# Performance work log

Measured on AMD Instinct MI355X. Metric: run time of the kernel, lower is better.

The kernel has to match this reference:

```python
import jax, jax.numpy as jnp
import numpy as np

NEG = -1.0e9


def setup_inputs() -> dict:
    key = jax.random.key(0)
    ks = jax.random.split(key, 8)
    B, L, D = 4, 2048, 1024
    s = 1.0 / np.sqrt(D)
    return {
        "x": jax.random.normal(ks[0], (B, L, D), dtype=jnp.float32),
        "Wq": jax.random.normal(ks[1], (D, D), dtype=jnp.float32) * s,
        "bq": jax.random.normal(ks[2], (D,), dtype=jnp.float32) * 0.02,
        "Wk": jax.random.normal(ks[3], (D, D), dtype=jnp.float32) * s,
        "bk": jax.random.normal(ks[4], (D,), dtype=jnp.float32) * 0.02,
        "Wv": jax.random.normal(ks[5], (D, D), dtype=jnp.float32) * s,
        "bv": jax.random.normal(ks[6], (D,), dtype=jnp.float32) * 0.02,
        "lengths": jax.random.randint(ks[7], (B,), 1, 2048, dtype=jnp.int32),
    }


def reference(x, Wq, bq, Wk, bk, Wv, bv, lengths):
    # x: [B, L, D]; single-head self-attention with causal + length additive masks
    B, L, D = x.shape
    q = x @ Wq + bq  # [B, L, D]
    k = x @ Wk + bk
    v = x @ Wv + bv
    scale = 1.0 / jnp.sqrt(jnp.asarray(D, dtype=x.dtype))
    att = jnp.einsum("bid,bjd->bij", q, k) * scale  # [B, L, L]
    idx = jnp.arange(L)
    causal = jnp.where(idx[None, :] > idx[:, None], NEG, 0.0).astype(x.dtype)  # [L, L]
    # length mask: NEG where j >= len[b] or i >= len[b]
    invalid = (idx[None, :] >= lengths[:, None])  # [B, L]
    lenmask = jnp.where(invalid[:, :, None] | invalid[:, None, :], NEG, 0.0).astype(x.dtype)
    att = att + causal[None, :, :] + lenmask
    att = jax.nn.softmax(att, axis=-1)
    return jnp.einsum("bij,bjd->bid", att, v)
```

## Files before the change

### kernel.cpp

```cpp
#include <hip/hip_runtime.h>

#define NEGV (-1.0e9f)

typedef __bf16 bf16_t;
typedef __bf16 bf16x8 __attribute__((ext_vector_type(8)));
typedef __bf16 bf16x4 __attribute__((ext_vector_type(4)));
typedef float  f32x4  __attribute__((ext_vector_type(4)));

__device__ __forceinline__ void gld16(const void* g, void* l) {
    __builtin_amdgcn_global_load_lds(
        (const __attribute__((address_space(1))) void*)g,
        (__attribute__((address_space(3))) void*)l, 16, 0, 0);
}


#define MMR(ACC, AF, IB)                                                                     \
    ACC[IB][0] = __builtin_amdgcn_mfma_f32_16x16x32_bf16(AF, b0, ACC[IB][0], 0, 0, 0);       \
    ACC[IB][1] = __builtin_amdgcn_mfma_f32_16x16x32_bf16(AF, b1, ACC[IB][1], 0, 0, 0);       \
    ACC[IB][2] = __builtin_amdgcn_mfma_f32_16x16x32_bf16(AF, b2, ACC[IB][2], 0, 0, 0);       \
    ACC[IB][3] = __builtin_amdgcn_mfma_f32_16x16x32_bf16(AF, b3, ACC[IB][3], 0, 0, 0)

__device__ __forceinline__ void ml128x128(
    const bf16_t* __restrict__ A, const bf16_t* __restrict__ B,
    int ldA, int ldB, int nkt, char* smem, int tid, f32x4 acc[4][4])
{
    const int w = tid >> 6, lane = tid & 63;
    const int wm = w & 1, wn = w >> 1;
    const int l16 = lane & 15, quad = lane >> 4;

    const int g0 = 2 * (tid >> 3) + ((tid >> 2) & 1);
    const int c0 = ((tid & 3) ^ ((tid >> 3) & 3)) * 8;
    const bf16_t* pa0 = A + (size_t)g0 * ldA + c0;
    const bf16_t* pa1 = pa0 + (size_t)64 * ldA;
    const bf16_t* pb0 = B + (size_t)g0 * ldB + c0;
    const bf16_t* pb1 = pb0 + (size_t)64 * ldB;
    char* const stA = smem + (w << 10);
    char* const stB = smem + 24576 + (w << 10);

    const int rowo = (l16 >> 1) * 128 + (l16 & 1) * 64 + ((quad ^ ((l16 >> 1) & 3)) << 4);
    const char* rdA = smem + (wm << 12) + rowo;
    const char* rdB = smem + 24576 + (wn << 12) + rowo;

#define STG4(BO) do { gld16(pa0, stA + (BO)); gld16(pa1, stA + (BO) + 4096);   \
                      gld16(pb0, stB + (BO)); gld16(pb1, stB + (BO) + 4096);   \
                      pa0 += 32; pa1 += 32; pb0 += 32; pb1 += 32; } while (0)

    STG4(0);
    if (nkt > 1) {
        STG4(8192);
        asm volatile("s_waitcnt vmcnt(4)" ::: "memory");
    } else {
        asm volatile("s_waitcnt vmcnt(0)" ::: "memory");
    }
    __builtin_amdgcn_s_barrier();

    int ro = 0, so = 16384;
    for (int kt = 0; kt < nkt; ++kt) {
        const char* ra = rdA + ro;
        const char* rb = rdB + ro;
        bf16x8 a0 = *(const bf16x8*)(ra);
        bf16x8 a1 = *(const bf16x8*)(ra + 1024);
        bf16x8 a2 = *(const bf16x8*)(ra + 2048);
        bf16x8 a3 = *(const bf16x8*)(ra + 3072);
        bf16x8 b0 = *(const bf16x8*)(rb);
        bf16x8 b1 = *(const bf16x8*)(rb + 1024);
        bf16x8 b2 = *(const bf16x8*)(rb + 2048);
        bf16x8 b3 = *(const bf16x8*)(rb + 3072);
        const bool st = (kt + 2) < nkt;
        if (st) STG4(so);
        asm volatile("s_waitcnt lgkmcnt(0)" ::: "memory");
        __builtin_amdgcn_sched_barrier(0);
        __builtin_amdgcn_s_setprio(1);
        MMR(acc, a0, 0); MMR(acc, a1, 1); MMR(acc, a2, 2); MMR(acc, a3, 3);
        __builtin_amdgcn_s_setprio(0);
        if (st) asm volatile("s_waitcnt vmcnt(4)" ::: "memory");
        else    asm volatile("s_waitcnt vmcnt(0)" ::: "memory");
        __builtin_amdgcn_s_barrier();
        ro = (ro == 16384) ? 0 : (ro + 8192);
        so = (so == 16384) ? 0 : (so + 8192);
    }
#undef STG4
}

__global__ __launch_bounds__(256)
void prep_kernel(const float* __restrict__ x, bf16_t* __restrict__ xb,
                 const float* __restrict__ W0, const float* __restrict__ W1,
                 const float* __restrict__ W2, bf16_t* __restrict__ WT)
{
    __shared__ float t[32][33];
    const int bid = blockIdx.x;
    if (bid < 4096) {
        const size_t i = ((size_t)bid * 256 + threadIdx.x) * 8;
        float4 a = *(const float4*)&x[i];
        float4 b = *(const float4*)&x[i + 4];
        bf16x8 o;
        o[0] = (bf16_t)a.x; o[1] = (bf16_t)a.y; o[2] = (bf16_t)a.z; o[3] = (bf16_t)a.w;
        o[4] = (bf16_t)b.x; o[5] = (bf16_t)b.y; o[6] = (bf16_t)b.z; o[7] = (bf16_t)b.w;
        *(bf16x8*)&xb[i] = o;
    } else {
        const int rr = bid - 4096;
        const int z = rr >> 10;
        const int rem = rr & 1023;
        const float* W = (z == 0) ? W0 : (z == 1) ? W1 : W2;
        bf16_t* WTz = WT + (size_t)z * 1024 * 1024;
        const int k0 = (rem >> 5) * 32, n0 = (rem & 31) * 32;
        const int r = threadIdx.x >> 3, c4 = (threadIdx.x & 7) * 4;
        float4 v = *(const float4*)&W[(size_t)(k0 + r) * 1024 + n0 + c4];
        t[r][c4 + 0] = v.x; t[r][c4 + 1] = v.y; t[r][c4 + 2] = v.z; t[r][c4 + 3] = v.w;
        __syncthreads();
        bf16x4 o;
#pragma unroll
        for (int j = 0; j < 4; ++j) o[j] = (bf16_t)t[c4 + j][r];
        *(bf16x4*)&WTz[(size_t)(n0 + r) * 1024 + k0 + c4] = o;
    }
}

__global__ __launch_bounds__(256)
void proj_kernel(const bf16_t* __restrict__ xb, const bf16_t* __restrict__ WT,
                 const float* __restrict__ bq, const float* __restrict__ bk,
                 const float* __restrict__ bv,
                 bf16_t* __restrict__ QK, bf16_t* __restrict__ VT,
                 int N2, int M, int Kd)
{
    __shared__ __align__(16) char smem[49152];
    const int tid = threadIdx.x;
    f32x4 acc[4][4];
#pragma unroll
    for (int i = 0; i < 4; ++i)
#pragma unroll
        for (int j = 0; j < 4; ++j) acc[i][j] = (f32x4)(0.0f);

    const int w = tid >> 6, lane = tid & 63;
    const int wm = w & 1, wn = w >> 1, quad = lane >> 4, l16 = lane & 15;

    if ((int)blockIdx.x < 1024) {
        int bid = blockIdx.x;
        bid = (bid & 7) * 128 + (bid >> 3);
        const int n0 = (bid & 15) << 7;
        const int m0 = (bid >> 4) << 7;
        ml128x128(xb + (size_t)m0 * Kd, WT + (size_t)n0 * Kd, Kd, Kd, Kd >> 5,
                  smem, tid, acc);
#pragma unroll
        for (int j = 0; j < 4; ++j) {
            const int col = n0 + wn * 64 + j * 16 + l16;
            const float bval = (col < 1024) ? bq[col] : bk[col - 1024];
#pragma unroll
            for (int i = 0; i < 4; ++i) {
                const int row = m0 + wm * 64 + i * 16 + quad * 4;
#pragma unroll
                for (int r = 0; r < 4; ++r)
                    QK[(size_t)(row + r) * N2 + col] = (bf16_t)(acc[i][j][r] + bval);
            }
        }
    } else {
        int bid = blockIdx.x - 1024;
        bid = (bid & 7) * 64 + (bid >> 3);
        const int m0 = (bid >> 6) << 7;
        const int n0 = (bid & 63) << 7;
        ml128x128(WT + (size_t)2 * Kd * Kd + (size_t)m0 * Kd,
                  xb + (size_t)n0 * Kd, Kd, Kd, Kd >> 5, smem, tid, acc);
#pragma unroll
        for (int i = 0; i < 4; ++i) {
            const int row = m0 + wm * 64 + i * 16 + quad * 4;
#pragma unroll
            for (int r = 0; r < 4; ++r) {
                const float bval = bv[row + r];
#pragma unroll
                for (int j = 0; j < 4; ++j) {
                    const int col = n0 + wn * 64 + j * 16 + l16;
                    VT[(size_t)(row + r) * M + col] = (bf16_t)(acc[i][j][r] + bval);
                }
            }
        }
    }
}

__global__ __launch_bounds__(256)
void scores128(const bf16_t* __restrict__ Q, const bf16_t* __restrict__ K,
               int ldq, const int* __restrict__ lengths,
               bf16_t* __restrict__ U, float* __restrict__ stats,
               int L, int Dd, float alpha)
{
    __shared__ __align__(16) char smem[49152];
    const int b = blockIdx.z;
    const int len = lengths[b];
    int tix = (int)blockIdx.x;
    tix = (tix & 7) * 17 + (tix >> 3);
    int it = 0;
    while ((it + 1) * (it + 2) / 2 <= tix) ++it;
    const int jt = tix - it * (it + 1) / 2;
    const int m0 = it << 7, n0 = jt << 7;
    const int tid = threadIdx.x;

    f32x4 acc[4][4];
#pragma unroll
    for (int i = 0; i < 4; ++i)
#pragma unroll
        for (int j = 0; j < 4; ++j) acc[i][j] = (f32x4)(0.0f);

    const bf16_t* Qb = Q + (size_t)b * L * ldq + (size_t)m0 * ldq;
    const bf16_t* Kb = K + (size_t)b * L * ldq + (size_t)n0 * ldq;
    ml128x128(Qb, Kb, ldq, ldq, Dd >> 5, smem, tid, acc);

    const int w = tid >> 6, lane = tid & 63;
    const int wm = w & 1, wn = w >> 1, quad = lane >> 4, l16 = lane & 15;
    bf16_t* Ub = U + (size_t)b * L * L;
    float* strow = stats + (size_t)b * L * 32;
    const int chnk = (n0 >> 6) + wn;
#pragma unroll
    for (int i = 0; i < 4; ++i) {
#pragma unroll
        for (int r = 0; r < 4; ++r) {
            const int row = m0 + wm * 64 + i * 16 + quad * 4 + r;
            float sv[4];
            float ssum = 0.f;
#pragma unroll
            for (int j = 0; j < 4; ++j) {
                const int col = n0 + wn * 64 + j * 16 + l16;
                float v = acc[i][j][r] * alpha;
                if (row >= len) v = (col > row) ? NEGV : 0.0f;
                else if (col > row || col >= len) v = NEGV;
                sv[j] = __expf(v - 8.0f);
                ssum += sv[j];
            }
            ssum += __shfl_xor(ssum, 1, 64);
            ssum += __shfl_xor(ssum, 2, 64);
            ssum += __shfl_xor(ssum, 4, 64);
            ssum += __shfl_xor(ssum, 8, 64);
#pragma unroll
            for (int j = 0; j < 4; ++j)
                Ub[(size_t)row * L + n0 + wn * 64 + j * 16 + l16] = (bf16_t)sv[j];
            if (l16 == 0) strow[(size_t)row * 32 + chnk] = ssum;
        }
    }
}

__global__ __launch_bounds__(256)
void pv128(const bf16_t* __restrict__ U, int ldp,
           const float* __restrict__ stats,
           const bf16_t* __restrict__ VT, int ldv,
           float* __restrict__ O, int L, int Dd)
{
    __shared__ __align__(16) char smem[49152];
    __shared__ float invD[128];
    const int b = blockIdx.z;
    const int bid = blockIdx.y * 8 + blockIdx.x;
    const int mt = 15 - (bid >> 3);
    const int m0 = mt << 7, n0 = (bid & 7) << 7;
    const int tid = threadIdx.x;

    {
        const int row = tid >> 1;
        const int half = tid & 1;
        const int nch = (m0 + 128) >> 6;
        const float* st = stats + ((size_t)b * L + m0 + row) * 32 + half * 16;
        float d = 0.f;
#pragma unroll
        for (int c = 0; c < 16; ++c) {
            const int ch = half * 16 + c;
            if (ch < nch) d += st[c];
        }
        d += __shfl_xor(d, 1, 64);
        if (half == 0) invD[row] = 1.0f / d;
    }
    __syncthreads();

    f32x4 acc[4][4];
#pragma unroll
    for (int i = 0; i < 4; ++i)
#pragma unroll
        for (int j = 0; j < 4; ++j) acc[i][j] = (f32x4)(0.0f);

    const int nkt = (m0 + 128) >> 5;
    const bf16_t* Pb = U + (size_t)b * L * ldp + (size_t)m0 * ldp;
    const bf16_t* Vb = VT + (size_t)b * L + (size_t)n0 * ldv;
    ml128x128(Pb, Vb, ldp, ldv, nkt, smem, tid, acc);

    float* Ob = O + (size_t)b * L * Dd;
    const int w = tid >> 6, lane = tid & 63;
    const int wm = w & 1, wn = w >> 1, quad = lane >> 4, l16 = lane & 15;
#pragma unroll
    for (int i = 0; i < 4; ++i) {
        const int rl = wm * 64 + i * 16 + quad * 4;
        const int row = m0 + rl;
#pragma unroll
        for (int r = 0; r < 4; ++r) {
            const float s = invD[rl + r];
#pragma unroll
            for (int j = 0; j < 4; ++j) {
                const int col = n0 + wn * 64 + j * 16 + l16;
                Ob[(size_t)(row + r) * Dd + col] = acc[i][j][r] * s;
            }
        }
    }
}

extern "C" void kernel_launch(void* const* d_in, const int* in_sizes, int n_in,
                              void* d_out, int out_size, void* d_ws, size_t ws_size,
                              hipStream_t stream)
{
    const float* x  = (const float*)d_in[0];
    const float* Wq = (const float*)d_in[1];
    const float* bq = (const float*)d_in[2];
    const float* Wk = (const float*)d_in[3];
    const float* bk = (const float*)d_in[4];
    const float* Wv = (const float*)d_in[5];
    const float* bv = (const float*)d_in[6];
    const int*  len = (const int*)d_in[7];
    float* out = (float*)d_out;

    const int B = 4, L = 2048, D = 1024;
    const int M = B * L;
    const int N2 = 2 * D;

    bf16_t* xb = (bf16_t*)d_ws;
    bf16_t* WT = xb + (size_t)M * D;
    bf16_t* QK = WT + (size_t)3 * D * D;
    bf16_t* VT = QK + (size_t)M * N2;
    bf16_t* U  = VT + (size_t)D * M;
    float* stats = (float*)(U + (size_t)B * L * L);

    prep_kernel<<<7168, 256, 0, stream>>>(x, xb, Wq, Wk, Wv, WT);

    proj_kernel<<<1536, 256, 0, stream>>>(xb, WT, bq, bk, bv, QK, VT, N2, M, D);

    scores128<<<dim3(136, 1, B), 256, 0, stream>>>(
        QK, QK + 1024, N2, len, U, stats, L, D, 0.03125f);

    pv128<<<dim3(8, 16, 4), 256, 0, stream>>>(U, L, stats, VT, M, out, L, D);
}
```

Measured before the change: 239.9 us.

## Skip attention tiles beyond sequence length; compute padded rows via prefix means

The scores kernel now returns early for tiles whose row or column start lies past the batch length. The PV kernel limits its K loop and stats reduction to valid columns and skips blocks and rows past the length. A new block row fills padded output rows with a running prefix mean of V, which is what the all-masked softmax reduces to under the causal mask. This avoids matmul and exp work on fully masked regions, but relies on that closed form and adds a serial column scan in the extra blocks.

```diff
diff --git a/kernel.cpp b/kernel.cpp
--- a/kernel.cpp
+++ b/kernel.cpp
@@ -190,6 +190,7 @@
     while ((it + 1) * (it + 2) / 2 <= tix) ++it;
     const int jt = tix - it * (it + 1) / 2;
     const int m0 = it << 7, n0 = jt << 7;
+    if (m0 >= len || n0 >= len) return;
     const int tid = threadIdx.x;
 
     f32x4 acc[4][4];
@@ -237,22 +238,44 @@
 
 __global__ __launch_bounds__(256)
 void pv128(const bf16_t* __restrict__ U, int ldp,
-           const float* __restrict__ stats,
+           const float* __restrict__ stats, const int* __restrict__ lengths,
            const bf16_t* __restrict__ VT, int ldv,
            float* __restrict__ O, int L, int Dd)
 {
     __shared__ __align__(16) char smem[49152];
     __shared__ float invD[128];
     const int b = blockIdx.z;
-    const int bid = blockIdx.y * 8 + blockIdx.x;
+    const int len = lengths[b];
+    const int tid = threadIdx.x;
+
+    if (blockIdx.y == 0) {
+        if (tid < 128) {
+            const int d = ((int)blockIdx.x << 7) + tid;
+            const bf16_t* vp = VT + (size_t)d * ldv + (size_t)b * L;
+            float* Ob = O + (size_t)b * L * Dd + d;
+            float cum = 0.f;
+            for (int l0 = 0; l0 < L; l0 += 8) {
+                bf16x8 v8 = *(const bf16x8*)(vp + l0);
+#pragma unroll
+                for (int j = 0; j < 8; ++j) {
+                    cum += (float)v8[j];
+                    const int l = l0 + j;
+                    if (l >= len) Ob[(size_t)l * Dd] = cum / (float)(l + 1);
+                }
+            }
+        }
+        return;
+    }
+
+    const int bid = ((int)blockIdx.y - 1) * 8 + blockIdx.x;
     const int mt = 15 - (bid >> 3);
     const int m0 = mt << 7, n0 = (bid & 7) << 7;
-    const int tid = threadIdx.x;
+    if (m0 >= len) return;
 
     {
         const int row = tid >> 1;
         const int half = tid & 1;
-        const int nch = (m0 + 128) >> 6;
+        const int nch = min((m0 + 128) >> 6, (len + 63) >> 6);
         const float* st = stats + ((size_t)b * L + m0 + row) * 32 + half * 16;
         float d = 0.f;
 #pragma unroll
@@ -271,7 +294,8 @@
 #pragma unroll
         for (int j = 0; j < 4; ++j) acc[i][j] = (f32x4)(0.0f);
 
-    const int nkt = (m0 + 128) >> 5;
+    const int kmax = min(m0 + 128, (len + 31) & ~31);
+    const int nkt = kmax >> 5;
     const bf16_t* Pb = U + (size_t)b * L * ldp + (size_t)m0 * ldp;
     const bf16_t* Vb = VT + (size_t)b * L + (size_t)n0 * ldv;
     ml128x128(Pb, Vb, ldp, ldv, nkt, smem, tid, acc);
@@ -285,6 +309,7 @@
         const int row = m0 + rl;
 #pragma unroll
         for (int r = 0; r < 4; ++r) {
+            if (row + r >= len) continue;
             const float s = invD[rl + r];
 #pragma unroll
             for (int j = 0; j < 4; ++j) {
@@ -327,5 +352,6 @@
     scores128<<<dim3(136, 1, B), 256, 0, stream>>>(
         QK, QK + 1024, N2, len, U, stats, L, D, 0.03125f);
 
-    pv128<<<dim3(8, 16, 4), 256, 0, stream>>>(U, L, stats, VT, M, out, L, D);
-}
+    pv128<<<dim3(8, 17, 4), 256, 0, stream>>>(
+        U, L, stats, len, VT, M, out, L, D);
+}
```

After: 319.6 us. 1.33x slower.
